# Kernel tuning notes

Measured on AMD Instinct MI355X. Metric: run time of the kernel, lower is better.

The kernel has to match this reference:

```python
import jax, jax.numpy as jnp
import numpy as np

D = 1024            # hidden dim (rows of classifier weight)
N_CLASSES = 50000   # number of SNOMED labels (columns)
G = 128             # number of meta-category groups
CLUSTER_PARAM = (1.0, 0.5, 0.5)  # config['cluster_param']


def setup_inputs() -> dict:
    key = jax.random.key(0)
    k1, k2 = jax.random.split(key)
    softmax_weight = jax.random.normal(k1, (D, N_CLASSES), dtype=jnp.float32) * 0.02
    group_ids = jax.random.randint(k2, (N_CLASSES,), 0, G)  # meta-group id per class
    return {"softmax_weight": softmax_weight, "group_ids": group_ids, "batch_size": 32}


def reference(softmax_weight, group_ids, batch_size):
    W = softmax_weight                      # [d, n_classes]
    n = W.shape[1]
    w_bar = W.sum(axis=1) / n               # [d] global column mean
    omega_mean = jnp.sum(W * W)             # ||W||_F^2

    # segmented per-group column sums and counts (one fused pass over W)
    counts = jax.ops.segment_sum(jnp.ones((n,), W.dtype), group_ids, num_segments=G)  # [G]
    sums = jax.ops.segment_sum(W.T, group_ids, num_segments=G)                         # [G, d]
    safe_counts = jnp.maximum(counts, 1.0)  # guard empty groups (contribute 0)
    w_c_bar = sums / safe_counts[:, None]   # [G, d] group means

    # omega_between = sum_c m_c * ||w_c_bar - w_bar||^2
    diff_b = w_c_bar - w_bar[None, :]
    omega_between = jnp.sum(counts * jnp.sum(diff_b * diff_b, axis=1))

    # omega_within = sum_i ||W[:, i] - w_c_bar[group(i)]||^2
    centered = W.T - w_c_bar[group_ids]     # [n_classes, d]
    omega_within = jnp.sum(centered * centered)

    bs = jnp.asarray(batch_size, W.dtype)
    return (omega_mean * CLUSTER_PARAM[0]
            + (omega_between * CLUSTER_PARAM[1] + omega_within * CLUSTER_PARAM[2]) / bs)
```

## Files before the change

kernel.cpp:

```cpp
#include <hip/hip_runtime.h>


#define D_ROWS 1024
#define N_CLS  50000
#define NVEC   (N_CLS / 4)

__global__ __launch_bounds__(256) void cluster_row_reduce(
    const float* __restrict__ W,
    float* __restrict__ row_sum,
    float* __restrict__ row_sq)
{
    const int row = blockIdx.x;
    const float4* __restrict__ Wrow =
        reinterpret_cast<const float4*>(W + (size_t)row * N_CLS);

    float s = 0.0f, q = 0.0f;
    for (int i = threadIdx.x; i < NVEC; i += 256) {
        float4 v = Wrow[i];
        s += v.x + v.y + v.z + v.w;
        q += v.x * v.x + v.y * v.y + v.z * v.z + v.w * v.w;
    }

    #pragma unroll
    for (int off = 32; off > 0; off >>= 1) {
        s += __shfl_down(s, off, 64);
        q += __shfl_down(q, off, 64);
    }

    __shared__ float ss[4], sq[4];
    const int wid  = threadIdx.x >> 6;
    const int lane = threadIdx.x & 63;
    if (lane == 0) { ss[wid] = s; sq[wid] = q; }
    __syncthreads();
    if (threadIdx.x == 0) {
        row_sum[row] = ss[0] + ss[1] + ss[2] + ss[3];
        row_sq[row]  = sq[0] + sq[1] + sq[2] + sq[3];
    }
}

__global__ __launch_bounds__(256) void cluster_final_reduce(
    const float* __restrict__ row_sum,
    const float* __restrict__ row_sq,
    const int* __restrict__ bs_ptr,
    float* __restrict__ out)
{
    float t2 = 0.0f, f = 0.0f;
    for (int i = threadIdx.x; i < D_ROWS; i += 256) {
        float rs = row_sum[i];
        t2 += rs * rs;
        f  += row_sq[i];
    }

    #pragma unroll
    for (int off = 32; off > 0; off >>= 1) {
        t2 += __shfl_down(t2, off, 64);
        f  += __shfl_down(f, off, 64);
    }

    __shared__ float st[4], sf[4];
    const int wid  = threadIdx.x >> 6;
    const int lane = threadIdx.x & 63;
    if (lane == 0) { st[wid] = t2; sf[wid] = f; }
    __syncthreads();
    if (threadIdx.x == 0) {
        float T2 = st[0] + st[1] + st[2] + st[3];
        float F  = sf[0] + sf[1] + sf[2] + sf[3];
        float bs = (float)bs_ptr[0];
        out[0] = F + 0.5f * (F - T2 / (float)N_CLS) / bs;
    }
}

extern "C" void kernel_launch(void* const* d_in, const int* in_sizes, int n_in,
                              void* d_out, int out_size, void* d_ws, size_t ws_size,
                              hipStream_t stream) {
    const float* W      = (const float*)d_in[0];
    const int*   bs_ptr = (const int*)d_in[2];
    float*       out    = (float*)d_out;

    float* row_sum = (float*)d_ws;
    float* row_sq  = row_sum + D_ROWS;

    cluster_row_reduce<<<D_ROWS, 256, 0, stream>>>(W, row_sum, row_sq);
    cluster_final_reduce<<<1, 256, 0, stream>>>(row_sum, row_sq, bs_ptr, out);
}
```

Before: 37.00 us.

## Fuse final reduction via last-block atomic counter and split rows in two

Merges the row-reduction and final-reduction kernels into one launch. The last block to finish, detected with an atomic counter and threadfence, performs the final combine. Each row is also split across two blocks, doubling the grid to 2048 blocks for better load balance across CUs. This removes a kernel launch and the gap between kernels, at the cost of an atomic per block. The counter is never reset but relies on modulo wraparound, so it depends on workspace starting at zero or a multiple of NBLK.

Result: slower. 83.42 us (+125.4%).

```diff
diff --git a/kernel.cpp b/kernel.cpp
--- a/kernel.cpp
+++ b/kernel.cpp
@@ -4,62 +4,74 @@
 #define D_ROWS 1024
 #define N_CLS  50000
 #define NVEC   (N_CLS / 4)
+#define PARTS  2
+#define CHUNK  (NVEC / PARTS)
+#define NBLK   (D_ROWS * PARTS)
 
-__global__ __launch_bounds__(256) void cluster_row_reduce(
+__global__ __launch_bounds__(256) void cluster_fused(
     const float* __restrict__ W,
-    float* __restrict__ row_sum,
-    float* __restrict__ row_sq)
+    const int* __restrict__ bs_ptr,
+    float* __restrict__ out,
+    float* __restrict__ sum_part,
+    float* __restrict__ sq_part,
+    unsigned int* __restrict__ counter)
 {
-    const int row = blockIdx.x;
-    const float4* __restrict__ Wrow =
-        reinterpret_cast<const float4*>(W + (size_t)row * N_CLS);
+    const int b    = blockIdx.x;
+    const int row  = b >> 1;
+    const int part = b & 1;
+    const float4* __restrict__ Wp =
+        reinterpret_cast<const float4*>(W + (size_t)row * N_CLS) + part * CHUNK;
 
     float s = 0.0f, q = 0.0f;
-    for (int i = threadIdx.x; i < NVEC; i += 256) {
-        float4 v = Wrow[i];
-        s += v.x + v.y + v.z + v.w;
+    for (int i = threadIdx.x; i < CHUNK; i += 256) {
+        float4 v = Wp[i];
+        s += (v.x + v.y) + (v.z + v.w);
         q += v.x * v.x + v.y * v.y + v.z * v.z + v.w * v.w;
     }
 
     #pragma unroll
-    for (int off = 32; off > 0; off >>= 1) {
+    for (int off = 32; off; off >>= 1) {
         s += __shfl_down(s, off, 64);
         q += __shfl_down(q, off, 64);
     }
 
     __shared__ float ss[4], sq[4];
+    __shared__ bool amLast;
     const int wid  = threadIdx.x >> 6;
     const int lane = threadIdx.x & 63;
     if (lane == 0) { ss[wid] = s; sq[wid] = q; }
     __syncthreads();
+
     if (threadIdx.x == 0) {
-        row_sum[row] = ss[0] + ss[1] + ss[2] + ss[3];
-        row_sq[row]  = sq[0] + sq[1] + sq[2] + sq[3];
+        sum_part[b] = ss[0] + ss[1] + ss[2] + ss[3];
+        sq_part[b]  = sq[0] + sq[1] + sq[2] + sq[3];
+        __threadfence();
+        unsigned int old = atomicAdd(counter, 1u);
+        amLast = ((old & (NBLK - 1)) == (NBLK - 1));
     }
-}
+    __syncthreads();
+    if (!amLast) return;
 
-__global__ __launch_bounds__(256) void cluster_final_reduce(
-    const float* __restrict__ row_sum,
-    const float* __restrict__ row_sq,
-    const int* __restrict__ bs_ptr,
-    float* __restrict__ out)
-{
+    __threadfence();
+
     float t2 = 0.0f, f = 0.0f;
-    for (int i = threadIdx.x; i < D_ROWS; i += 256) {
-        float rs = row_sum[i];
-        t2 += rs * rs;
-        f  += row_sq[i];
+    {
+        volatile const float* vs = sum_part;
+        volatile const float* vq = sq_part;
+        for (int r = threadIdx.x; r < D_ROWS; r += 256) {
+            float rs = vs[2 * r] + vs[2 * r + 1];
+            t2 += rs * rs;
+            f  += vq[2 * r] + vq[2 * r + 1];
+        }
     }
 
     #pragma unroll
-    for (int off = 32; off > 0; off >>= 1) {
+    for (int off = 32; off; off >>= 1) {
         t2 += __shfl_down(t2, off, 64);
         f  += __shfl_down(f, off, 64);
     }
 
     __shared__ float st[4], sf[4];
-    const int wid  = threadIdx.x >> 6;
-    const int lane = threadIdx.x & 63;
     if (lane == 0) { st[wid] = t2; sf[wid] = f; }
     __syncthreads();
     if (threadIdx.x == 0) {
@@ -77,9 +89,9 @@
     const int*   bs_ptr = (const int*)d_in[2];
     float*       out    = (float*)d_out;
 
-    float* row_sum = (float*)d_ws;
-    float* row_sq  = row_sum + D_ROWS;
+    float*        sum_part = (float*)d_ws;
+    float*        sq_part  = sum_part + NBLK;
+    unsigned int* counter  = (unsigned int*)(sq_part + NBLK);
 
-    cluster_row_reduce<<<D_ROWS, 256, 0, stream>>>(W, row_sum, row_sq);
-    cluster_final_reduce<<<1, 256, 0, stream>>>(row_sum, row_sq, bs_ptr, out);
+    cluster_fused<<<NBLK, 256, 0, stream>>>(W, bs_ptr, out, sum_part, sq_part, counter);
 }
```
